# Kernel tuning notes

Measured on AMD Instinct MI355X. Metric: run time of the kernel, lower is better.

The kernel has to match this reference:

```python
import jax, jax.numpy as jnp
import numpy as np

WIN, OFFSET_D, TRUNC, SIGMA = 60, 40, 21, 9
EPS = 1e-8


def smoothing_filter():
    half = TRUNC // 2
    x = jnp.arange(-half, half + 1, dtype=jnp.float32)
    g = jnp.exp(-0.5 * (x / SIGMA) ** 2)
    g = g / g.sum()
    f = jnp.zeros(WIN, jnp.float32)
    c = WIN // 2
    return f.at[c - half:c + half + 1].set(g)


def setup_inputs() -> dict:
    key = jax.random.key(0)
    kx, kl, kt, kw = jax.random.split(key, 4)
    B, T, K = 64, 4000, 100
    X = jax.random.uniform(kx, (B, T, K), jnp.float32, 1e-4, 1.0 - 1e-4)
    lengths = jax.random.randint(kl, (B,), T // 2, T + 1, dtype=jnp.int32)
    tgt = jax.random.randint(kt, (B,), 0, K, dtype=jnp.int32)
    w_end = jax.random.randint(kw, (B,), 1, T // 2, dtype=jnp.int32)
    return {"X": X, "lengths": lengths, "tgt": tgt, "w_end": w_end}


def reference(X, lengths, tgt, w_end):
    B, T, K = X.shape
    filt = smoothing_filter()
    tau_s = jnp.maximum(0, w_end + OFFSET_D - WIN)      # (B,)
    tau_e = jnp.minimum(tau_s + WIN, lengths)           # (B,)
    t = jnp.arange(T)

    # ---- negative term: -log(1 - p) over all valid frames, excluding the
    # target keyword's pooling window [tau_s, tau_e) ----
    neg = -jnp.log(jnp.clip(1.0 - X, EPS, 1.0))                         # (B,T,K)
    len_mask = (t[None, :] < lengths[:, None]).astype(X.dtype)          # (B,T)
    win_mask = ((t[None, :] >= tau_s[:, None]) & (t[None, :] < tau_e[:, None])).astype(X.dtype)
    tgt_onehot = jax.nn.one_hot(tgt, K, dtype=X.dtype)                  # (B,K)
    neg_loss = jnp.sum(neg * len_mask[:, :, None]) - jnp.einsum('btk,bt,bk->', neg, win_mask, tgt_onehot)

    # ---- positive term: smoothed max pooling over window of target keyword ----
    prob_tgt = jnp.take_along_axis(X, tgt[:, None, None], axis=2)[..., 0]  # (B,T)
    win = jax.vmap(lambda p, s: jax.lax.dynamic_slice(p, (s,), (WIN,)))(prob_tgt, tau_s)
    Lw = tau_e - tau_s                                                   # valid window length
    pos = jnp.arange(WIN)
    valid = pos[None, :] < Lw[:, None]
    win = win * valid.astype(X.dtype)  # zero beyond valid length == zero-padded ragged conv
    total_pad = WIN - 1
    pl = total_pad // 2  # torch 'same': extra pad on the right
    smoothed = jax.lax.conv_general_dilated(
        win[:, None, :], filt[None, None, :], (1,), [(pl, total_pad - pl)])[:, 0, :]
    smoothed = jnp.clip(smoothed, EPS, 1.0)
    smoothed = jnp.where(valid, smoothed, 0.0)  # exclude out-of-window positions from max
    pos_loss = -jnp.log(smoothed.max(axis=1)).sum()

    return neg_loss + pos_loss
```

## Files before the change

### kernel.cpp

```cpp
#include <hip/hip_runtime.h>

#define WIN      60
#define OFFSET_D 40
#define TRUNC    21
#define EPS      1e-8f
#define BB       64
#define TT       4000
#define KK       100
#define TK       (TT*KK)
#define CH       50
#define CHUNK    (TK/CH)
#define NB1      (BB*CH)
#define NPART    (NB1 + BB)

__global__ __launch_bounds__(256) void fused_kernel(const float* __restrict__ X,
                                                    const int* __restrict__ lengths,
                                                    const int* __restrict__ tgt,
                                                    const int* __restrict__ w_end,
                                                    double* __restrict__ partials) {
    const int bid = blockIdx.x;

    if (bid < NB1) {
        const int b    = bid / CH;
        const int c    = bid - b * CH;
        const int s    = c * CHUNK;
        const int lenK = lengths[b] * KK;
        const int e    = min(s + CHUNK, lenK);

        const float* __restrict__ base = X + (size_t)b * TK;
        float a0 = 0.f, a1 = 0.f, a2 = 0.f, a3 = 0.f;

        #pragma unroll 4
        for (int m = s + (threadIdx.x << 2); m < e; m += 256 * 4) {
            const float4 v = *reinterpret_cast<const float4*>(base + m);
            a0 -= __logf(fminf(fmaxf(1.0f - v.x, EPS), 1.0f));
            a1 -= __logf(fminf(fmaxf(1.0f - v.y, EPS), 1.0f));
            a2 -= __logf(fminf(fmaxf(1.0f - v.z, EPS), 1.0f));
            a3 -= __logf(fminf(fmaxf(1.0f - v.w, EPS), 1.0f));
        }
        float local = (a0 + a1) + (a2 + a3);

        #pragma unroll
        for (int off = 32; off > 0; off >>= 1) local += __shfl_down(local, off);
        __shared__ float wsum[4];
        if ((threadIdx.x & 63) == 0) wsum[threadIdx.x >> 6] = local;
        __syncthreads();
        if (threadIdx.x == 0)
            partials[bid] = (double)(wsum[0] + wsum[1] + wsum[2] + wsum[3]);
        return;
    }

    if (threadIdx.x >= 64) return;
    const int b   = bid - NB1;
    const int tid = threadIdx.x;

    const int ts = max(0, w_end[b] + OFFSET_D - WIN);
    const int te = min(ts + WIN, lengths[b]);
    const int Lw = te - ts;
    const int tg = tgt[b];

    float g = 0.0f;
    if (tid < TRUNC) {
        const float x = (tid - 10) * (1.0f / 9.0f);
        g = __expf(-0.5f * x * x);
    }
    float gs = g;
    #pragma unroll
    for (int off = 32; off > 0; off >>= 1) gs += __shfl_down(gs, off);
    gs = __shfl(gs, 0);
    const float gnorm = g / gs;

    float w = 0.0f, sub = 0.0f;
    if (tid < Lw) {
        const float xw = X[(size_t)b * TK + (size_t)(ts + tid) * KK + tg];
        w = xw;
        sub = -__logf(fminf(fmaxf(1.0f - xw, EPS), 1.0f));
    }

    float sm = 0.0f;
    #pragma unroll
    for (int u = 0; u < TRUNC; ++u) {
        const float gu = __shfl(gnorm, u);
        const int   j  = tid - 9 + u;
        const float wv = __shfl(w, j & 63);
        sm += gu * (((unsigned)j < (unsigned)WIN) ? wv : 0.0f);
    }

    float cand = (tid < Lw) ? fminf(fmaxf(sm, EPS), 1.0f) : 0.0f;
    #pragma unroll
    for (int off = 32; off > 0; off >>= 1) {
        sub  += __shfl_down(sub, off);
        cand  = fmaxf(cand, __shfl_down(cand, off));
    }
    if (tid == 0)
        partials[NB1 + b] = (double)(-__logf(cand) - sub);
}

__global__ __launch_bounds__(256) void finalize_kernel(const double* __restrict__ p,
                                                       float* __restrict__ out) {
    double s = 0.0;
    for (int i = threadIdx.x; i < NPART; i += 256) s += p[i];
    #pragma unroll
    for (int off = 32; off > 0; off >>= 1) s += __shfl_down(s, off);
    __shared__ double wsum[4];
    if ((threadIdx.x & 63) == 0) wsum[threadIdx.x >> 6] = s;
    __syncthreads();
    if (threadIdx.x == 0)
        out[0] = (float)(wsum[0] + wsum[1] + wsum[2] + wsum[3]);
}

extern "C" void kernel_launch(void* const* d_in, const int* in_sizes, int n_in,
                              void* d_out, int out_size, void* d_ws, size_t ws_size,
                              hipStream_t stream) {
    const float* X        = (const float*)d_in[0];
    const int*   lengths  = (const int*)d_in[1];
    const int*   tgt      = (const int*)d_in[2];
    const int*   w_end    = (const int*)d_in[3];
    float*       out      = (float*)d_out;
    double*      partials = (double*)d_ws;

    fused_kernel<<<NB1 + BB, 256, 0, stream>>>(X, lengths, tgt, w_end, partials);
    finalize_kernel<<<1, 256, 0, stream>>>(partials, out);
}
```

Before: 153.6 us.

## Replace per-element logs with log of products and batch chunk loads

Each thread now multiplies four clamped (1-x) values and takes a single log, which cuts the number of transcendental ops by four. Chunks become fixed 8192-element blocks whose full-chunk path issues eight float4 loads up front for more memory-level parallelism. Tail and out-of-length chunks take a fallback loop or skip the work entirely. The window blocks move to the front of the grid. A product of four values each clamped near 1e-8 could underflow, which risks precision loss in extreme cases.

After: 152.1 us. About the same (-1.0%).

```diff
diff --git a/kernel.cpp b/kernel.cpp
--- a/kernel.cpp
+++ b/kernel.cpp
@@ -8,10 +8,13 @@
 #define TT       4000
 #define KK       100
 #define TK       (TT*KK)
-#define CH       50
-#define CHUNK    (TK/CH)
-#define NB1      (BB*CH)
-#define NPART    (NB1 + BB)
+#define CHUNK    8192
+#define CHB      49
+#define NPART    (BB + BB*CHB)
+
+__device__ __forceinline__ float clamp1(float x) {
+    return fminf(fmaxf(1.0f - x, EPS), 1.0f);
+}
 
 __global__ __launch_bounds__(256) void fused_kernel(const float* __restrict__ X,
                                                     const int* __restrict__ lengths,
@@ -20,23 +23,37 @@
                                                     double* __restrict__ partials) {
     const int bid = blockIdx.x;
 
-    if (bid < NB1) {
-        const int b    = bid / CH;
-        const int c    = bid - b * CH;
+    if (bid >= BB) {
+        const int nb   = bid - BB;
+        const int b    = nb / CHB;
+        const int c    = nb - b * CHB;
         const int s    = c * CHUNK;
         const int lenK = lengths[b] * KK;
-        const int e    = min(s + CHUNK, lenK);
+        const float* __restrict__ base = X + (size_t)b * TK;
 
-        const float* __restrict__ base = X + (size_t)b * TK;
         float a0 = 0.f, a1 = 0.f, a2 = 0.f, a3 = 0.f;
 
-        #pragma unroll 4
-        for (int m = s + (threadIdx.x << 2); m < e; m += 256 * 4) {
-            const float4 v = *reinterpret_cast<const float4*>(base + m);
-            a0 -= __logf(fminf(fmaxf(1.0f - v.x, EPS), 1.0f));
-            a1 -= __logf(fminf(fmaxf(1.0f - v.y, EPS), 1.0f));
-            a2 -= __logf(fminf(fmaxf(1.0f - v.z, EPS), 1.0f));
-            a3 -= __logf(fminf(fmaxf(1.0f - v.w, EPS), 1.0f));
+        if (s + CHUNK <= lenK) {
+            const float* __restrict__ p = base + s + (threadIdx.x << 2);
+            float4 v[8];
+            #pragma unroll
+            for (int k = 0; k < 8; ++k)
+                v[k] = *reinterpret_cast<const float4*>(p + k * 1024);
+            #pragma unroll
+            for (int k = 0; k < 8; ++k) {
+                const float pr = (clamp1(v[k].x) * clamp1(v[k].y)) *
+                                 (clamp1(v[k].z) * clamp1(v[k].w));
+                ((k & 3) == 0 ? a0 : (k & 3) == 1 ? a1 : (k & 3) == 2 ? a2 : a3)
+                    -= __logf(pr);
+            }
+        } else if (s < lenK) {
+            const int e = min(s + CHUNK, lenK);
+            for (int m = s + (threadIdx.x << 2); m < e; m += 256 * 4) {
+                const float4 v = *reinterpret_cast<const float4*>(base + m);
+                const float pr = (clamp1(v.x) * clamp1(v.y)) *
+                                 (clamp1(v.z) * clamp1(v.w));
+                a0 -= __logf(pr);
+            }
         }
         float local = (a0 + a1) + (a2 + a3);
 
@@ -51,7 +68,7 @@
     }
 
     if (threadIdx.x >= 64) return;
-    const int b   = bid - NB1;
+    const int b   = bid;
     const int tid = threadIdx.x;
 
     const int ts = max(0, w_end[b] + OFFSET_D - WIN);
@@ -74,7 +91,7 @@
     if (tid < Lw) {
         const float xw = X[(size_t)b * TK + (size_t)(ts + tid) * KK + tg];
         w = xw;
-        sub = -__logf(fminf(fmaxf(1.0f - xw, EPS), 1.0f));
+        sub = -__logf(clamp1(xw));
     }
 
     float sm = 0.0f;
@@ -93,7 +110,7 @@
         cand  = fmaxf(cand, __shfl_down(cand, off));
     }
     if (tid == 0)
-        partials[NB1 + b] = (double)(-__logf(cand) - sub);
+        partials[bid] = (double)(-__logf(cand) - sub);
 }
 
 __global__ __launch_bounds__(256) void finalize_kernel(const double* __restrict__ p,
@@ -119,6 +136,6 @@
     float*       out      = (float*)d_out;
     double*      partials = (double*)d_ws;
 
-    fused_kernel<<<NB1 + BB, 256, 0, stream>>>(X, lengths, tgt, w_end, partials);
+    fused_kernel<<<BB + BB * CHB, 256, 0, stream>>>(X, lengths, tgt, w_end, partials);
     finalize_kernel<<<1, 256, 0, stream>>>(partials, out);
 }
```
